# Kernel optimization log

Measured on AMD Instinct MI355X. Metric: run time of the kernel, lower is better.

Reference implementation:

```python
import jax, jax.numpy as jnp
import numpy as np

DT = 0.001  # seconds per step (keras_spiking default)
BATCH, SEQ, SIZE = 64, 1024, 512


def setup_inputs() -> dict:
    key = jax.random.key(0)
    k1, k2 = jax.random.split(key)
    inputs = jax.random.normal(k1, (BATCH, SEQ, SIZE), dtype=jnp.float32)
    initial_level = jnp.zeros((SIZE,), dtype=jnp.float32)
    # time constants around the 0.01s used in the docstring example
    tau = 0.005 + 0.05 * jax.random.uniform(k2, (SIZE,), dtype=jnp.float32)
    return {"inputs": inputs, "initial_level": initial_level, "tau": tau}


def _alpha_filter(inputs, initial_level, tau):
    # inputs: [B, T, K]; initial_level, tau: [K]
    B_, T, K = inputs.shape
    tau_c = jnp.maximum(tau, 1e-8)               # clip for stability (as in forward pass)
    dt_tau = DT / tau_c                           # [K]
    dt_tau2 = dt_tau / tau_c                      # [K]
    e = jnp.exp(-dt_tau)                          # [K]
    # per-feature 2x2 transition matrix A: [K, 2, 2]
    row0 = jnp.stack([1.0 - dt_tau, -dt_tau2], axis=-1)             # [K, 2]
    row1 = jnp.stack([DT * jnp.ones_like(tau_c), 1.0 + dt_tau], -1)  # [K, 2]
    A = e[:, None, None] * jnp.stack([row0, row1], axis=-2)          # [K, 2, 2]
    # input vector B: [K, 2]
    Bvec = jnp.stack([e * dt_tau2, 1.0 - e * (1.0 + dt_tau)], axis=-1)
    Bt = Bvec.T  # [2, K]
    # initial state: row 0 zeros, row 1 initial_level -> [B, 2, K]
    x0 = jnp.stack(
        [jnp.zeros((B_, K), inputs.dtype),
         jnp.broadcast_to(initial_level, (B_, K))], axis=1)

    def step(x, u):
        # x: [B, 2, K], u: [B, K]
        xn = jnp.einsum('kij,mjk->mik', A, x) + Bt[None, :, :] * u[:, None, :]
        return xn, xn[:, 1]  # output is second state component

    _, ys = jax.lax.scan(step, x0, jnp.swapaxes(inputs, 0, 1))  # ys: [T, B, K]
    return jnp.swapaxes(ys, 0, 1)  # [B, T, K]


def reference(inputs, initial_level, tau):
    return _alpha_filter(inputs, initial_level, tau)
```

## Files before the change

### kernel.cpp

```cpp
#include <hip/hip_runtime.h>
#include <math.h>

namespace {
constexpr int kB  = 64;
constexpr int kT  = 1024;
constexpr int kK  = 512;
constexpr int kC  = 8;
constexpr int kL  = kT / kC;
constexpr int kKB = 64;
constexpr int kPF = 8;
constexpr float kDT = 0.001f;
}

__global__ __launch_bounds__(kKB * kC, 4) void alpha_scan2(
    const float* __restrict__ in,
    const float* __restrict__ init_level,
    const float* __restrict__ tau,
    float* __restrict__ out)
{
    __shared__ float sF0[kC][kKB];
    __shared__ float sF1[kC][kKB];

    const int lane = threadIdx.x & 63;
    const int c    = threadIdx.x >> 6;
    const int kg   = blockIdx.x & 7;
    const int b    = blockIdx.x >> 3;
    const int k    = kg * kKB + lane;

    const float tc      = fmaxf(tau[k], 1e-8f);
    const float dt_tau  = kDT / tc;
    const float dt_tau2 = dt_tau / tc;
    const float e       = expf(-dt_tau);

    const float a00 = e * (1.0f - dt_tau);
    const float a01 = e * (-dt_tau2);
    const float a10 = e * kDT;
    const float a11 = e * (1.0f + dt_tau);
    const float b0  = e * dt_tau2;
    const float b1  = 1.0f - e * (1.0f + dt_tau);

    const float* __restrict__ pin =
        in + ((size_t)b * kT + (size_t)c * kL) * kK + k;

    float x0 = 0.0f, x1 = 0.0f;
    {
        float buf[kPF];
        #pragma unroll
        for (int i = 0; i < kPF; ++i) buf[i] = pin[(size_t)i * kK];
        for (int t0 = 0; t0 < kL - kPF; t0 += kPF) {
            const float* __restrict__ pld = pin + (size_t)(t0 + kPF) * kK;
            #pragma unroll
            for (int i = 0; i < kPF; ++i) {
                const float u = buf[i];
                buf[i] = pld[(size_t)i * kK];
                const float n0 = fmaf(a00, x0, fmaf(a01, x1, b0 * u));
                const float n1 = fmaf(a10, x0, fmaf(a11, x1, b1 * u));
                x0 = n0; x1 = n1;
            }
        }
        #pragma unroll
        for (int i = 0; i < kPF; ++i) {
            const float u = buf[i];
            const float n0 = fmaf(a00, x0, fmaf(a01, x1, b0 * u));
            const float n1 = fmaf(a10, x0, fmaf(a11, x1, b1 * u));
            x0 = n0; x1 = n1;
        }
    }
    sF0[c][lane] = x0;
    sF1[c][lane] = x1;
    __syncthreads();

    float m00 = a00, m01 = a01, m10 = a10, m11 = a11;
    #pragma unroll
    for (int s = 0; s < 7; ++s) {
        const float t00 = fmaf(m00, m00, m01 * m10);
        const float t01 = fmaf(m00, m01, m01 * m11);
        const float t10 = fmaf(m10, m00, m11 * m10);
        const float t11 = fmaf(m10, m01, m11 * m11);
        m00 = t00; m01 = t01; m10 = t10; m11 = t11;
    }

    float s0 = 0.0f, s1 = init_level[k];
    for (int cp = 0; cp < c; ++cp) {
        const float f0 = sF0[cp][lane];
        const float f1 = sF1[cp][lane];
        const float n0 = fmaf(m00, s0, fmaf(m01, s1, f0));
        const float n1 = fmaf(m10, s0, fmaf(m11, s1, f1));
        s0 = n0; s1 = n1;
    }

    x0 = s0; x1 = s1;
    float* __restrict__ pout =
        out + ((size_t)b * kT + (size_t)c * kL) * kK + k;
    {
        float buf[kPF];
        #pragma unroll
        for (int i = 0; i < kPF; ++i) buf[i] = pin[(size_t)i * kK];
        for (int t0 = 0; t0 < kL - kPF; t0 += kPF) {
            const float* __restrict__ pld = pin  + (size_t)(t0 + kPF) * kK;
            float* __restrict__ pst       = pout + (size_t)t0 * kK;
            #pragma unroll
            for (int i = 0; i < kPF; ++i) {
                const float u = buf[i];
                buf[i] = pld[(size_t)i * kK];
                const float n0 = fmaf(a00, x0, fmaf(a01, x1, b0 * u));
                const float n1 = fmaf(a10, x0, fmaf(a11, x1, b1 * u));
                x0 = n0; x1 = n1;
                pst[(size_t)i * kK] = n1;
            }
        }
        float* __restrict__ pst = pout + (size_t)(kL - kPF) * kK;
        #pragma unroll
        for (int i = 0; i < kPF; ++i) {
            const float u = buf[i];
            const float n0 = fmaf(a00, x0, fmaf(a01, x1, b0 * u));
            const float n1 = fmaf(a10, x0, fmaf(a11, x1, b1 * u));
            x0 = n0; x1 = n1;
            pst[(size_t)i * kK] = n1;
        }
    }
}

extern "C" void kernel_launch(void* const* d_in, const int* in_sizes, int n_in,
                              void* d_out, int out_size, void* d_ws, size_t ws_size,
                              hipStream_t stream) {
    const float* in  = (const float*)d_in[0];
    const float* il  = (const float*)d_in[1];
    const float* tau = (const float*)d_in[2];
    float* out = (float*)d_out;

    dim3 block(kKB * kC);
    dim3 grid(kB * (kK / kKB));
    alpha_scan2<<<grid, block, 0, stream>>>(in, il, tau, out);
}
```

Before: 253.8 us.

## Keep each chunk's inputs in registers and split time into 16 chunks

Doubles the number of time chunks per block to 16, so each thread handles 64 steps, and loads the whole chunk's inputs into a register array once. Both scan passes then reuse those registers, so the input is read from global memory once instead of twice. The matrix-power loop is shortened to match the new chunk length. The cost is a large register footprint per thread (64 floats plus state) with 1024-thread blocks, which risks spills or lower occupancy.

Result: no change. 257.4 us (+1.4%).

```diff
diff --git a/kernel.cpp b/kernel.cpp
--- a/kernel.cpp
+++ b/kernel.cpp
@@ -5,14 +5,13 @@
 constexpr int kB  = 64;
 constexpr int kT  = 1024;
 constexpr int kK  = 512;
-constexpr int kC  = 8;
+constexpr int kC  = 16;
 constexpr int kL  = kT / kC;
 constexpr int kKB = 64;
-constexpr int kPF = 8;
 constexpr float kDT = 0.001f;
 }
 
-__global__ __launch_bounds__(kKB * kC, 4) void alpha_scan2(
+__global__ __launch_bounds__(kKB * kC, 4) void alpha_scan3(
     const float* __restrict__ in,
     const float* __restrict__ init_level,
     const float* __restrict__ tau,
@@ -42,29 +41,16 @@
     const float* __restrict__ pin =
         in + ((size_t)b * kT + (size_t)c * kL) * kK + k;
 
+    float u[kL];
+    #pragma unroll
+    for (int t = 0; t < kL; ++t) u[t] = pin[(size_t)t * kK];
+
     float x0 = 0.0f, x1 = 0.0f;
-    {
-        float buf[kPF];
-        #pragma unroll
-        for (int i = 0; i < kPF; ++i) buf[i] = pin[(size_t)i * kK];
-        for (int t0 = 0; t0 < kL - kPF; t0 += kPF) {
-            const float* __restrict__ pld = pin + (size_t)(t0 + kPF) * kK;
-            #pragma unroll
-            for (int i = 0; i < kPF; ++i) {
-                const float u = buf[i];
-                buf[i] = pld[(size_t)i * kK];
-                const float n0 = fmaf(a00, x0, fmaf(a01, x1, b0 * u));
-                const float n1 = fmaf(a10, x0, fmaf(a11, x1, b1 * u));
-                x0 = n0; x1 = n1;
-            }
-        }
-        #pragma unroll
-        for (int i = 0; i < kPF; ++i) {
-            const float u = buf[i];
-            const float n0 = fmaf(a00, x0, fmaf(a01, x1, b0 * u));
-            const float n1 = fmaf(a10, x0, fmaf(a11, x1, b1 * u));
-            x0 = n0; x1 = n1;
-        }
+    #pragma unroll
+    for (int t = 0; t < kL; ++t) {
+        const float n0 = fmaf(a00, x0, fmaf(a01, x1, b0 * u[t]));
+        const float n1 = fmaf(a10, x0, fmaf(a11, x1, b1 * u[t]));
+        x0 = n0; x1 = n1;
     }
     sF0[c][lane] = x0;
     sF1[c][lane] = x1;
@@ -72,7 +58,7 @@
 
     float m00 = a00, m01 = a01, m10 = a10, m11 = a11;
     #pragma unroll
-    for (int s = 0; s < 7; ++s) {
+    for (int s = 0; s < 6; ++s) {
         const float t00 = fmaf(m00, m00, m01 * m10);
         const float t01 = fmaf(m00, m01, m01 * m11);
         const float t10 = fmaf(m10, m00, m11 * m10);
@@ -92,32 +78,12 @@
     x0 = s0; x1 = s1;
     float* __restrict__ pout =
         out + ((size_t)b * kT + (size_t)c * kL) * kK + k;
-    {
-        float buf[kPF];
-        #pragma unroll
-        for (int i = 0; i < kPF; ++i) buf[i] = pin[(size_t)i * kK];
-        for (int t0 = 0; t0 < kL - kPF; t0 += kPF) {
-            const float* __restrict__ pld = pin  + (size_t)(t0 + kPF) * kK;
-            float* __restrict__ pst       = pout + (size_t)t0 * kK;
-            #pragma unroll
-            for (int i = 0; i < kPF; ++i) {
-                const float u = buf[i];
-                buf[i] = pld[(size_t)i * kK];
-                const float n0 = fmaf(a00, x0, fmaf(a01, x1, b0 * u));
-                const float n1 = fmaf(a10, x0, fmaf(a11, x1, b1 * u));
-                x0 = n0; x1 = n1;
-                pst[(size_t)i * kK] = n1;
-            }
-        }
-        float* __restrict__ pst = pout + (size_t)(kL - kPF) * kK;
-        #pragma unroll
-        for (int i = 0; i < kPF; ++i) {
-            const float u = buf[i];
-            const float n0 = fmaf(a00, x0, fmaf(a01, x1, b0 * u));
-            const float n1 = fmaf(a10, x0, fmaf(a11, x1, b1 * u));
-            x0 = n0; x1 = n1;
-            pst[(size_t)i * kK] = n1;
-        }
+    #pragma unroll
+    for (int t = 0; t < kL; ++t) {
+        const float n0 = fmaf(a00, x0, fmaf(a01, x1, b0 * u[t]));
+        const float n1 = fmaf(a10, x0, fmaf(a11, x1, b1 * u[t]));
+        x0 = n0; x1 = n1;
+        pout[(size_t)t * kK] = n1;
     }
 }
 
@@ -131,5 +97,5 @@
 
     dim3 block(kKB * kC);
     dim3 grid(kB * (kK / kKB));
-    alpha_scan2<<<grid, block, 0, stream>>>(in, il, tau, out);
+    alpha_scan3<<<grid, block, 0, stream>>>(in, il, tau, out);
 }
```
